# Performance work log

Hardware: AMD Instinct MI355X
Metric: run time of the kernel (lower is better)

The kernel has to match this reference:

```python
import jax, jax.numpy as jnp
import numpy as np
import math

B, L, M = 8, 1024, 1024
H, D, DK, DFF = 16, 1024, 64, 4096
EPS = 1e-5


def _ln(x, g, b):
    mu = jnp.mean(x, axis=-1, keepdims=True)
    var = jnp.mean((x - mu) ** 2, axis=-1, keepdims=True)
    return (x - mu) * jax.lax.rsqrt(var + EPS) * g + b


def _mha(x, kv, Wq, bq, Wk, bk, Wv, bv, Wo, bo, masked):
    # x: [B,Lq,D], kv: [B,Lk,D]; per-head weights stacked: Wq [H,D,DK], bq [H,DK]
    Q = jnp.einsum('bld,hdk->bhlk', x, Wq) + bq[None, :, None, :]
    K = jnp.einsum('bld,hdk->bhlk', kv, Wk) + bk[None, :, None, :]
    V = jnp.einsum('bld,hdk->bhlk', kv, Wv) + bv[None, :, None, :]
    scores = jnp.einsum('bhqk,bhmk->bhqm', Q, K) / math.sqrt(DK)
    p = jax.nn.softmax(scores, axis=-1)
    if masked:
        # faithful to source: mask applied AFTER softmax (multiply by tril ones)
        Lq = x.shape[1]
        tril = jnp.tril(jnp.ones((Lq, kv.shape[1]), dtype=p.dtype))
        p = p * tril
    z = jnp.einsum('bhqm,bhmk->bhqk', p, V)  # [B,H,Lq,DK]
    z = jnp.transpose(z, (0, 2, 1, 3)).reshape(x.shape[0], x.shape[1], H * DK)
    return z @ Wo + bo


def _forward(x, enc, Wq1, bq1, Wk1, bk1, Wv1, bv1, Wo1, bo1,
             Wq2, bq2, Wk2, bk2, Wv2, bv2, Wo2, bo2,
             W1, b1, W2, b2, g1, be1, g2, be2, g3, be3):
    z = _mha(x, x, Wq1, bq1, Wk1, bk1, Wv1, bv1, Wo1, bo1, masked=True)
    x = _ln(z + x, g1, be1)
    z = _mha(x, enc, Wq2, bq2, Wk2, bk2, Wv2, bv2, Wo2, bo2, masked=False)
    x = _ln(z + x, g2, be2)
    # Conv1d(k=1) pair == per-token MLP: relu(x @ W1 + b1) @ W2 + b2
    y = jax.nn.relu(x @ W1 + b1) @ W2 + b2
    return _ln(y + x, g3, be3)


def setup_inputs() -> dict:
    key = jax.random.key(0)
    ks = jax.random.split(key, 16)
    s = 0.02
    return {
        'x': jax.random.normal(ks[0], (B, L, D), jnp.float32),
        'enc': jax.random.normal(ks[1], (B, M, D), jnp.float32),
        'Wq1': jax.random.normal(ks[2], (H, D, DK), jnp.float32) * s,
        'bq1': jnp.zeros((H, DK), jnp.float32),
        'Wk1': jax.random.normal(ks[3], (H, D, DK), jnp.float32) * s,
        'bk1': jnp.zeros((H, DK), jnp.float32),
        'Wv1': jax.random.normal(ks[4], (H, D, DK), jnp.float32) * s,
        'bv1': jnp.zeros((H, DK), jnp.float32),
        'Wo1': jax.random.normal(ks[5], (H * DK, D), jnp.float32) * s,
        'bo1': jnp.zeros((D,), jnp.float32),
        'Wq2': jax.random.normal(ks[6], (H, D, DK), jnp.float32) * s,
        'bq2': jnp.zeros((H, DK), jnp.float32),
        'Wk2': jax.random.normal(ks[7], (H, D, DK), jnp.float32) * s,
        'bk2': jnp.zeros((H, DK), jnp.float32),
        'Wv2': jax.random.normal(ks[8], (H, D, DK), jnp.float32) * s,
        'bv2': jnp.zeros((H, DK), jnp.float32),
        'Wo2': jax.random.normal(ks[9], (H * DK, D), jnp.float32) * s,
        'bo2': jnp.zeros((D,), jnp.float32),
        'W1': jax.random.normal(ks[10], (D, DFF), jnp.float32) * s,
        'b1': jnp.zeros((DFF,), jnp.float32),
        'W2': jax.random.normal(ks[11], (DFF, D), jnp.float32) * s,
        'b2': jnp.zeros((D,), jnp.float32),
        'g1': jnp.ones((D,), jnp.float32), 'be1': jnp.zeros((D,), jnp.float32),
        'g2': jnp.ones((D,), jnp.float32), 'be2': jnp.zeros((D,), jnp.float32),
        'g3': jnp.ones((D,), jnp.float32), 'be3': jnp.zeros((D,), jnp.float32),
    }


def reference(x, enc, Wq1, bq1, Wk1, bk1, Wv1, bv1, Wo1, bo1,
              Wq2, bq2, Wk2, bk2, Wv2, bv2, Wo2, bo2,
              W1, b1, W2, b2, g1, be1, g2, be2, g3, be3):
    return _forward(x, enc, Wq1, bq1, Wk1, bk1, Wv1, bv1, Wo1, bo1,
                    Wq2, bq2, Wk2, bk2, Wv2, bv2, Wo2, bo2,
                    W1, b1, W2, b2, g1, be1, g2, be2, g3, be3)
```

## Files before the change

kernel.cpp:

```cpp
#include <hip/hip_runtime.h>
#include <hip/hip_bf16.h>

typedef __bf16 bf16;
typedef __bf16 bf16x8 __attribute__((ext_vector_type(8)));
typedef __bf16 bf16x4v __attribute__((ext_vector_type(4)));
typedef float f32x4 __attribute__((ext_vector_type(4)));
typedef unsigned int u32;
typedef u32 u32x4 __attribute__((ext_vector_type(4)));

#define DEV static __device__ __forceinline__
#define SB0 __builtin_amdgcn_sched_barrier(0)
#define BAR __builtin_amdgcn_s_barrier()
#define LGKM0 asm volatile("s_waitcnt lgkmcnt(0)" ::: "memory")
#define LGKM8 asm volatile("s_waitcnt lgkmcnt(8)" ::: "memory")
#define VM4 asm volatile("s_waitcnt vmcnt(4)" ::: "memory")
#define PRIO1 __builtin_amdgcn_s_setprio(1)
#define PRIO0 __builtin_amdgcn_s_setprio(0)

DEV void gll16(const void* g, void* l) {
  __builtin_amdgcn_global_load_lds((__attribute__((address_space(1))) void*)g,
                                   (__attribute__((address_space(3))) void*)l,
                                   16, 0, 0);
}

DEV bf16 tobf(float f) { return (bf16)f; }

DEV u32 cvtpk(float lo, float hi) {
  u32 r;
  asm("v_cvt_pk_bf16_f32 %0, %1, %2" : "=v"(r) : "v"(lo), "v"(hi));
  return r;
}

__global__ void cast_f2b_kernel(const float* __restrict__ in, bf16* __restrict__ out, int n4) {
  int i = blockIdx.x * 256 + threadIdx.x;
  if (i < n4) {
    const float4 v = ((const float4*)in)[i];
    bf16x4v o;
    o[0] = tobf(v.x); o[1] = tobf(v.y); o[2] = tobf(v.z); o[3] = tobf(v.w);
    ((bf16x4v*)out)[i] = o;
  }
}

__global__ __launch_bounds__(256)
void tpack_kernel(const float* __restrict__ in, bf16* __restrict__ out,
                  int K, int N, int in_hs, int out_hs, float scale) {
  __shared__ float tile[32][33];
  const int k0 = blockIdx.x << 5, n0 = blockIdx.y << 5;
  const float* ip = in + (size_t)blockIdx.z * in_hs;
  bf16* op = out + (size_t)blockIdx.z * out_hs;
  const int tx = threadIdx.x & 31, ty = threadIdx.x >> 5;
#pragma unroll
  for (int r = 0; r < 4; ++r)
    tile[ty * 4 + r][tx] = ip[(size_t)(k0 + ty * 4 + r) * N + n0 + tx];
  __syncthreads();
#pragma unroll
  for (int r = 0; r < 4; ++r)
    op[(size_t)(n0 + ty * 4 + r) * K + k0 + tx] = tobf(tile[tx][ty * 4 + r] * scale);
}

__global__ void bscale_kernel(const float* __restrict__ in, float* __restrict__ out, int n, float s) {
  int i = blockIdx.x * 256 + threadIdx.x;
  if (i < n) out[i] = in[i] * s;
}

template<int EPI>
__global__ __launch_bounds__(512, 1)
void gemm8(const bf16* __restrict__ A, const bf16* __restrict__ W,
           const float* __restrict__ bias, const float* __restrict__ resid,
           void* __restrict__ outv, int M, int N, int K) {
  __shared__ bf16 sA[3][256 * 64];
  __shared__ bf16 sB[3][128 * 64];
  const int nbx = N >> 7;
  const int nwg = (M >> 8) * nbx;
  int bid = (int)blockIdx.x;
  bid = (bid & 7) * (nwg >> 3) + (bid >> 3);
  const int tm = bid / nbx, tn = bid - tm * nbx;
  const int tid = threadIdx.x;
  const int lane = tid & 63;
  const int w = tid >> 6;
  const int wr = w >> 1, wc = w & 1;
  const int l15 = lane & 15, l4 = lane >> 4;

  const bf16* Abase = A + (size_t)(tm * 256) * K;
  const bf16* Bbase = W + (size_t)(tn * 128) * K;

  f32x4 acc[4][4] = {};
  const int nt = K >> 6;

  auto stageA = [&](int buf, int t) {
#pragma unroll
    for (int j = 0; j < 4; ++j) {
      int g = tid + (j << 9);
      int row = g >> 3;
      int sc = ((g & 7) ^ (row & 7)) << 3;
      gll16(Abase + (size_t)row * K + (t << 6) + sc, &sA[buf][g << 3]);
    }
  };
  auto stageB = [&](int buf, int t) {
#pragma unroll
    for (int j = 0; j < 2; ++j) {
      int g = tid + (j << 9);
      int row = g >> 3;
      int sc = ((g & 7) ^ (row & 7)) << 3;
      gll16(Bbase + (size_t)row * K + (t << 6) + sc, &sB[buf][g << 3]);
    }
  };

  stageA(0, 0); stageB(0, 0);
  stageA(1, 1 < nt ? 1 : 0); stageB(1, 1 < nt ? 1 : 0);
  SB0;
  asm volatile("s_waitcnt vmcnt(6)" ::: "memory");
  BAR;

  int c = 0;
  for (int t = 0; t < nt; ++t) {
    const int sb = (c >= 1) ? c - 1 : 2;
    const int ts = (t + 2 < nt) ? t + 2 : nt - 1;
    bf16x8 af[4][2], bfr[4][2];
#pragma unroll
    for (int mi = 0; mi < 4; ++mi)
#pragma unroll
      for (int kk = 0; kk < 2; ++kk) {
        int r = wr * 64 + (mi << 4) + l15;
        int off = (r << 7) + (kk << 6) + (l4 << 4);
        off ^= (r & 7) << 4;
        af[mi][kk] = *(const bf16x8*)((const char*)sA[c] + off);
      }
#pragma unroll
    for (int ni = 0; ni < 2; ++ni)
#pragma unroll
      for (int kk = 0; kk < 2; ++kk) {
        int r = wc * 64 + (ni << 4) + l15;
        int off = (r << 7) + (kk << 6) + (l4 << 4);
        off ^= (r & 7) << 4;
        bfr[ni][kk] = *(const bf16x8*)((const char*)sB[c] + off);
      }
    stageA(sb, ts);
    SB0; BAR; LGKM0; SB0; PRIO1;
#pragma unroll
    for (int mi = 0; mi < 4; ++mi)
#pragma unroll
      for (int ni = 0; ni < 2; ++ni)
#pragma unroll
        for (int kk = 0; kk < 2; ++kk)
          acc[mi][ni] = __builtin_amdgcn_mfma_f32_16x16x32_bf16(af[mi][kk], bfr[ni][kk],
                                                                acc[mi][ni], 0, 0, 0);
    PRIO0; SB0; BAR;
#pragma unroll
    for (int ni = 2; ni < 4; ++ni)
#pragma unroll
      for (int kk = 0; kk < 2; ++kk) {
        int r = wc * 64 + (ni << 4) + l15;
        int off = (r << 7) + (kk << 6) + (l4 << 4);
        off ^= (r & 7) << 4;
        bfr[ni][kk] = *(const bf16x8*)((const char*)sB[c] + off);
      }
    stageB(sb, ts);
    SB0;
    asm volatile("s_waitcnt vmcnt(6)" ::: "memory");
    BAR; LGKM0; SB0; PRIO1;
#pragma unroll
    for (int mi = 0; mi < 4; ++mi)
#pragma unroll
      for (int ni = 2; ni < 4; ++ni)
#pragma unroll
        for (int kk = 0; kk < 2; ++kk)
          acc[mi][ni] = __builtin_amdgcn_mfma_f32_16x16x32_bf16(af[mi][kk], bfr[ni][kk],
                                                                acc[mi][ni], 0, 0, 0);
    PRIO0; SB0; BAR;
    c = (c == 2) ? 0 : c + 1;
  }

  const int row0 = tm * 256 + wr * 64 + (l4 << 2);
  const int col0 = tn * 128 + wc * 64 + l15;
#pragma unroll
  for (int ni = 0; ni < 4; ++ni) {
    const int col = col0 + (ni << 4);
    const float bv = bias ? bias[col] : 0.f;
#pragma unroll
    for (int mi = 0; mi < 4; ++mi) {
      const int rr = row0 + (mi << 4);
      f32x4 v = acc[mi][ni];
      if (EPI == 0) {
        bf16* out = (bf16*)outv;
#pragma unroll
        for (int r = 0; r < 4; ++r) out[(size_t)(rr + r) * N + col] = tobf(v[r] + bv);
      } else if (EPI == 1) {
        float* out = (float*)outv;
#pragma unroll
        for (int r = 0; r < 4; ++r) {
          size_t idx = (size_t)(rr + r) * N + col;
          out[idx] = v[r] + bv + resid[idx];
        }
      }
    }
  }
}

template<int EPI>
__global__ __launch_bounds__(512, 1)
void gemmP(const bf16* __restrict__ A, const bf16* __restrict__ W,
           const float* __restrict__ bias, const float* __restrict__ resid,
           void* __restrict__ outv, int M, int N, int K) {
  __shared__ bf16 sA[2][2][128 * 64];
  __shared__ bf16 sB[2][2][128 * 64];
  const int nbx = N >> 8;
  const int nwg = (M >> 8) * nbx;
  int bid = (int)blockIdx.x;
  bid = (bid & 7) * (nwg >> 3) + (bid >> 3);
  const int tm = bid / nbx, tn = bid - tm * nbx;
  const int tid = threadIdx.x;
  const int lane = tid & 63;
  const int w = tid >> 6;
  const int wr = w >> 2, wc = w & 3;
  const int l15 = lane & 15, l4 = lane >> 4;

  const bf16* Abase = A + (size_t)(tm * 256) * K;
  const bf16* Bbase = W + (size_t)(tn * 256) * K;

  f32x4 acc[8][4] = {};
  const int nt = K >> 6;
  const int nit = nt >> 1;

  auto stageHalf = [&](const bf16* base, bf16* lds, int t, int h) {
#pragma unroll
    for (int j = 0; j < 2; ++j) {
      int g = tid + (j << 9);
      int row = g >> 3;
      int sc = ((g & 7) ^ (row & 7)) << 3;
      gll16(base + (size_t)(h * 128 + row) * K + (t << 6) + sc, &lds[g << 3]);
    }
  };
  auto rdoff = [&](int r, int kk) {
    int off = (r << 7) + (kk << 6) + (l4 << 4);
    return off ^ ((r & 7) << 4);
  };

  stageHalf(Abase, sA[0][0], 0, 0);
  stageHalf(Abase, sA[0][1], 0, 1);
  stageHalf(Bbase, sB[0][0], 0, 0);
  stageHalf(Bbase, sB[0][1], 0, 1);
  stageHalf(Bbase, sB[1][0], 1, 0);
  stageHalf(Bbase, sB[1][1], 1, 1);
  SB0; VM4; BAR;

  for (int it = 0; it < nit; ++it) {
    const int tod = 2 * it + 1;
    const int ts2 = (2 * it + 2 < nt) ? 2 * it + 2 : nt - 1;
    const int ts3 = (2 * it + 3 < nt) ? 2 * it + 3 : nt - 1;

    auto doTile = [&](int b, int ab, int at, int bb, int bt) {
      bf16x8 af[4][2], ag[4][2], b01[2][2], b23[2][2];
      const char* pA = (const char*)sA[b][wr];
      const char* pB = (const char*)sB[b][wc >> 1];
      const int brow = (wc & 1) << 6;
#pragma unroll
      for (int mi = 0; mi < 4; ++mi)
#pragma unroll
        for (int kk = 0; kk < 2; ++kk)
          af[mi][kk] = *(const bf16x8*)(pA + rdoff((mi << 4) + l15, kk));
#pragma unroll
      for (int ni = 0; ni < 2; ++ni)
#pragma unroll
        for (int kk = 0; kk < 2; ++kk)
          b01[ni][kk] = *(const bf16x8*)(pB + rdoff(brow + (ni << 4) + l15, kk));
      stageHalf(Abase, sA[ab][0], at, 0);
      SB0; LGKM8; BAR; LGKM0; SB0; PRIO1;
#pragma unroll
      for (int mi = 0; mi < 4; ++mi)
#pragma unroll
        for (int ni = 0; ni < 2; ++ni)
#pragma unroll
          for (int kk = 0; kk < 2; ++kk)
            acc[mi][ni] = __builtin_amdgcn_mfma_f32_16x16x32_bf16(af[mi][kk], b01[ni][kk],
                                                                  acc[mi][ni], 0, 0, 0);
      PRIO0; SB0; BAR;
#pragma unroll
      for (int ni = 0; ni < 2; ++ni)
#pragma unroll
        for (int kk = 0; kk < 2; ++kk)
          b23[ni][kk] = *(const bf16x8*)(pB + rdoff(brow + 32 + (ni << 4) + l15, kk));
      stageHalf(Abase, sA[ab][1], at, 1);
      SB0; BAR; LGKM0; SB0; PRIO1;
#pragma unroll
      for (int mi = 0; mi < 4; ++mi)
#pragma unroll
        for (int ni = 0; ni < 2; ++ni)
#pragma unroll
          for (int kk = 0; kk < 2; ++kk)
            acc[mi][ni + 2] = __builtin_amdgcn_mfma_f32_16x16x32_bf16(af[mi][kk], b23[ni][kk],
                                                                      acc[mi][ni + 2], 0, 0, 0);
      PRIO0; SB0; BAR;
#pragma unroll
      for (int mi = 0; mi < 4; ++mi)
#pragma unroll
        for (int kk = 0; kk < 2; ++kk)
          ag[mi][kk] = *(const bf16x8*)(pA + rdoff(64 + (mi << 4) + l15, kk));
      stageHalf(Bbase, sB[bb][0], bt, 0);
      SB0; BAR; LGKM0; SB0; PRIO1;
#pragma unroll
      for (int mi = 0; mi < 4; ++mi)
#pragma unroll
        for (int ni = 0; ni < 2; ++ni)
#pragma unroll
          for (int kk = 0; kk < 2; ++kk)
            acc[mi + 4][ni] = __builtin_amdgcn_mfma_f32_16x16x32_bf16(ag[mi][kk], b01[ni][kk],
                                                                      acc[mi + 4][ni], 0, 0, 0);
      PRIO0; SB0; BAR;
      stageHalf(Bbase, sB[bb][1], bt, 1);
      SB0; VM4; BAR; PRIO1;
#pragma unroll
      for (int mi = 0; mi < 4; ++mi)
#pragma unroll
        for (int ni = 0; ni < 2; ++ni)
#pragma unroll
          for (int kk = 0; kk < 2; ++kk)
            acc[mi + 4][ni + 2] = __builtin_amdgcn_mfma_f32_16x16x32_bf16(ag[mi][kk], b23[ni][kk],
                                                                          acc[mi + 4][ni + 2], 0, 0, 0);
      PRIO0; SB0; BAR;
    };

    doTile(0, 1, tod, 0, ts2);
    doTile(1, 0, ts2, 1, ts3);
  }

  const int row0 = tm * 256 + wr * 128 + (l4 << 2);
  const int col0 = tn * 256 + wc * 64 + l15;
#pragma unroll
  for (int ni = 0; ni < 4; ++ni) {
    const int col = col0 + (ni << 4);
    const float bv = bias ? bias[col] : 0.f;
#pragma unroll
    for (int mi = 0; mi < 8; ++mi) {
      const int rr = row0 + (mi << 4);
      f32x4 v = acc[mi][ni];
      if (EPI == 2) {
        bf16* out = (bf16*)outv;
#pragma unroll
        for (int r = 0; r < 4; ++r) out[(size_t)(rr + r) * N + col] = tobf(fmaxf(v[r] + bv, 0.f));
      } else {
        bf16* out = (bf16*)outv;
        const int seg = col >> 10;
        const int cc = col & 1023;
        const bool isV = (EPI == 4) ? (seg == 2) : (seg == 1);
        if (isV) {
          bf16* vout = out + (size_t)seg * 8388608;
          const int bb = rr >> 10, l0 = rr & 1023;
          const int hh = cc >> 6, dk = cc & 63;
          bf16x4v pk;
#pragma unroll
          for (int r = 0; r < 4; ++r) pk[r] = tobf(v[r] + bv);
          *(bf16x4v*)(vout + ((size_t)((bb * 16 + hh) * 64 + dk) << 10) + l0) = pk;
        } else {
          bf16* qout = out + (size_t)seg * 8388608;
#pragma unroll
          for (int r = 0; r < 4; ++r) qout[(size_t)(rr + r) * 1024 + cc] = tobf(v[r] + bv);
        }
      }
    }
  }
}

template<bool MASKED>
__global__ __launch_bounds__(256, 2)
void attn_kernel(const bf16* __restrict__ Qp, const bf16* __restrict__ Kp,
                 const bf16* __restrict__ Vt, bf16* __restrict__ Z) {
  __shared__ bf16 sK[2][64 * 64];
  __shared__ bf16 sV[2][64 * 64];
  const int Lk = 1024;
  const int d = blockIdx.x;
  const int bh = d & 127, qb = d >> 7;
  const int b = bh >> 4, h = bh & 15;
  const int q0 = qb << 7;
  const int tid = threadIdx.x, lane = tid & 63, w = tid >> 6;
  const int l15 = lane & 15, l4 = lane >> 4;

  const bf16* Qb = Qp + ((size_t)(b * 1024 + q0 + w * 32)) * 1024 + h * 64;
  bf16x8 qf[2][2];
#pragma unroll
  for (int mi = 0; mi < 2; ++mi)
#pragma unroll
    for (int kk = 0; kk < 2; ++kk)
      qf[mi][kk] = *(const bf16x8*)(Qb + (size_t)((mi << 4) + l15) * 1024 + (kk << 5) + (l4 << 3));

  f32x4 o[4][2] = {};
  float Mr[2] = {-1e30f, -1e30f}, LrP[2] = {0.f, 0.f};

  const bf16* Kb = Kp + ((size_t)b * Lk) * 1024 + h * 64;
  const bf16* Vb = Vt + ((size_t)(b * 16 + h)) * 64 * Lk;

  auto stage = [&](int buf, int t, bool withV) {
    const int kv0 = t << 6;
#pragma unroll
    for (int j = 0; j < 2; ++j) {
      int g = tid + (j << 8);
      int r = g >> 3;
      int sc = ((g & 7) ^ (r & 7)) << 3;
      gll16(Kb + (size_t)(kv0 + r) * 1024 + sc, &sK[buf][g << 3]);
      if (withV) gll16(Vb + (size_t)r * Lk + kv0 + sc, &sV[buf][g << 3]);
    }
  };
  auto needPV = [&](int t) -> bool { return !MASKED || ((t << 6) < q0 + 128); };

  const int NT = Lk >> 6;
  stage(0, 0, true);
  __syncthreads();
  int cur = 0;

  for (int t = 0; t < NT; ++t) {
    if (t + 1 < NT) stage(cur ^ 1, t + 1, needPV(t + 1));
    const int kv0 = t << 6;

    f32x4 s[4][2] = {};
#pragma unroll
    for (int n = 0; n < 4; ++n) {
      bf16x8 kf[2];
#pragma unroll
      for (int kk = 0; kk < 2; ++kk) {
        int r = (n << 4) + l15;
        int off = (r << 7) + (kk << 6) + (l4 << 4);
        off ^= (r & 7) << 4;
        kf[kk] = *(const bf16x8*)((const char*)sK[cur] + off);
      }
#pragma unroll
      for (int mi = 0; mi < 2; ++mi)
#pragma unroll
        for (int kk = 0; kk < 2; ++kk)
          s[n][mi] = __builtin_amdgcn_mfma_f32_16x16x32_bf16(kf[kk], qf[mi][kk],
                                                             s[n][mi], 0, 0, 0);
    }

#pragma unroll
    for (int mi = 0; mi < 2; ++mi) {
      float lmax = s[0][mi][0];
#pragma unroll
      for (int n = 0; n < 4; ++n)
#pragma unroll
        for (int r = 0; r < 4; ++r) lmax = fmaxf(lmax, s[n][mi][r]);
      const bool need = (t == 0) || !__all(lmax <= Mr[mi] + 8.f);
      if (need) {
        float tmx = fmaxf(lmax, __shfl_xor(lmax, 16, 64));
        tmx = fmaxf(tmx, __shfl_xor(tmx, 32, 64));
        const float Mn = fmaxf(Mr[mi], tmx);
        const float al = exp2f(Mr[mi] - Mn);
        LrP[mi] *= al;
        Mr[mi] = Mn;
#pragma unroll
        for (int r = 0; r < 4; ++r) {
          float a = __shfl(al, (l4 << 2) + r, 64);
#pragma unroll
          for (int nd = 0; nd < 4; ++nd) o[nd][mi][r] *= a;
        }
      }
      float rs = 0.f;
#pragma unroll
      for (int n = 0; n < 4; ++n)
#pragma unroll
        for (int r = 0; r < 4; ++r) {
          float p = exp2f(s[n][mi][r] - Mr[mi]);
          s[n][mi][r] = p;
          rs += p;
        }
      LrP[mi] += rs;
    }

    if (needPV(t)) {
      const bool needMask = MASKED && (kv0 + 63 > q0 + (w << 5));
      bf16x8 pa[2][2];
#pragma unroll
      for (int mi = 0; mi < 2; ++mi) {
        u32 D0[4], D1[4];
        const int qg = q0 + (w << 5) + (mi << 4) + l15;
#pragma unroll
        for (int n = 0; n < 4; ++n) {
          float pv[4];
#pragma unroll
          for (int r = 0; r < 4; ++r) {
            float p = s[n][mi][r];
            if (needMask) {
              int cg = kv0 + (n << 4) + (l4 << 2) + r;
              if (cg > qg) p = 0.f;
            }
            pv[r] = p;
          }
          D0[n] = cvtpk(pv[0], pv[1]);
          D1[n] = cvtpk(pv[2], pv[3]);
        }
        const int src = l15 + ((lane & 16) << 1);
#pragma unroll
        for (int kk = 0; kk < 2; ++kk) {
          u32 v0 = (lane & 32) ? D0[2 * kk + 1] : D0[2 * kk];
          u32 v1 = (lane & 32) ? D1[2 * kk + 1] : D1[2 * kk];
          u32x4 tw;
          tw[0] = (u32)__shfl((int)v0, src, 64);
          tw[1] = (u32)__shfl((int)v1, src, 64);
          tw[2] = (u32)__shfl((int)v0, src + 16, 64);
          tw[3] = (u32)__shfl((int)v1, src + 16, 64);
          pa[mi][kk] = __builtin_bit_cast(bf16x8, tw);
        }
      }
#pragma unroll
      for (int nd = 0; nd < 4; ++nd) {
        bf16x8 vf[2];
#pragma unroll
        for (int kk = 0; kk < 2; ++kk) {
          int r = (nd << 4) + l15;
          int off = (r << 7) + (kk << 6) + (l4 << 4);
          off ^= (r & 7) << 4;
          vf[kk] = *(const bf16x8*)((const char*)sV[cur] + off);
        }
#pragma unroll
        for (int mi = 0; mi < 2; ++mi)
#pragma unroll
          for (int kk = 0; kk < 2; ++kk)
            o[nd][mi] = __builtin_amdgcn_mfma_f32_16x16x32_bf16(pa[mi][kk], vf[kk],
                                                                o[nd][mi], 0, 0, 0);
      }
    }
    __syncthreads();
    cur ^= 1;
  }

  float inv[2][4];
#pragma unroll
  for (int mi = 0; mi < 2; ++mi) {
    float l = LrP[mi];
    l += __shfl_xor(l, 16, 64);
    l += __shfl_xor(l, 32, 64);
    const float il = 1.f / l;
#pragma unroll
    for (int r = 0; r < 4; ++r) inv[mi][r] = __shfl(il, (l4 << 2) + r, 64);
  }
  bf16* Zb = Z + ((size_t)(b * 1024 + q0 + w * 32)) * 1024 + h * 64;
#pragma unroll
  for (int nd = 0; nd < 4; ++nd)
#pragma unroll
    for (int mi = 0; mi < 2; ++mi)
#pragma unroll
      for (int r = 0; r < 4; ++r)
        Zb[(size_t)((mi << 4) + (l4 << 2) + r) * 1024 + (nd << 4) + l15] =
            tobf(o[nd][mi][r] * inv[mi][r]);
}

__global__ __launch_bounds__(256)
void ln_kernel(const float* __restrict__ in, const float* __restrict__ gw,
               const float* __restrict__ bw, float* __restrict__ outf,
               bf16* __restrict__ outb) {
  const int row = blockIdx.x, tid = threadIdx.x;
  const size_t base = (size_t)row << 10;
  const float4 v = *(const float4*)(in + base + tid * 4);
  float s = v.x + v.y + v.z + v.w;
  float ss = v.x * v.x + v.y * v.y + v.z * v.z + v.w * v.w;
#pragma unroll
  for (int d = 1; d < 64; d <<= 1) { s += __shfl_xor(s, d, 64); ss += __shfl_xor(ss, d, 64); }
  __shared__ float red[8];
  const int w = tid >> 6;
  if ((tid & 63) == 0) { red[w] = s; red[4 + w] = ss; }
  __syncthreads();
  s = red[0] + red[1] + red[2] + red[3];
  ss = red[4] + red[5] + red[6] + red[7];
  const float mu = s * (1.f / 1024.f);
  const float var = ss * (1.f / 1024.f) - mu * mu;
  const float rstd = rsqrtf(var + 1e-5f);
  const float4 g4 = *(const float4*)(gw + tid * 4);
  const float4 b4 = *(const float4*)(bw + tid * 4);
  const float o0 = (v.x - mu) * rstd * g4.x + b4.x;
  const float o1 = (v.y - mu) * rstd * g4.y + b4.y;
  const float o2 = (v.z - mu) * rstd * g4.z + b4.z;
  const float o3 = (v.w - mu) * rstd * g4.w + b4.w;
  if (outf) { float4 of; of.x = o0; of.y = o1; of.z = o2; of.w = o3;
              *(float4*)(outf + base + tid * 4) = of; }
  if (outb) { bf16x4v ob; ob[0] = tobf(o0); ob[1] = tobf(o1); ob[2] = tobf(o2); ob[3] = tobf(o3);
              *(bf16x4v*)(outb + base + tid * 4) = ob; }
}

extern "C" void kernel_launch(void* const* d_in, const int* in_sizes, int n_in,
                              void* d_out, int out_size, void* d_ws, size_t ws_size,
                              hipStream_t stream) {
  const float* x   = (const float*)d_in[0];
  const float* enc = (const float*)d_in[1];
  const float* Wq1 = (const float*)d_in[2];
  const float* bq1 = (const float*)d_in[3];
  const float* Wk1 = (const float*)d_in[4];
  const float* bk1 = (const float*)d_in[5];
  const float* Wv1 = (const float*)d_in[6];
  const float* bv1 = (const float*)d_in[7];
  const float* Wo1 = (const float*)d_in[8];
  const float* bo1 = (const float*)d_in[9];
  const float* Wq2 = (const float*)d_in[10];
  const float* bq2 = (const float*)d_in[11];
  const float* Wk2 = (const float*)d_in[12];
  const float* bk2 = (const float*)d_in[13];
  const float* Wv2 = (const float*)d_in[14];
  const float* bv2 = (const float*)d_in[15];
  const float* Wo2 = (const float*)d_in[16];
  const float* bo2 = (const float*)d_in[17];
  const float* W1  = (const float*)d_in[18];
  const float* b1  = (const float*)d_in[19];
  const float* W2  = (const float*)d_in[20];
  const float* b2  = (const float*)d_in[21];
  const float* g1  = (const float*)d_in[22];
  const float* be1 = (const float*)d_in[23];
  const float* g2  = (const float*)d_in[24];
  const float* be2 = (const float*)d_in[25];
  const float* g3  = (const float*)d_in[26];
  const float* be3 = (const float*)d_in[27];

  char* ws = (char*)d_ws;
  size_t off = 0;
  auto alloc = [&](size_t bytes) { char* p = ws + off; off += (bytes + 255) & ~(size_t)255; return p; };
  const size_t ACT = (size_t)8 * 1024 * 1024 * 2;
  const float QSC = 0.125f * 1.44269504088896f;

  bf16* xb     = (bf16*)alloc(ACT);
  bf16* encb   = (bf16*)alloc(ACT);
  bf16* Wqkv1t = (bf16*)alloc((size_t)3072 * 1024 * 2);
  bf16* Wkv2t  = (bf16*)alloc((size_t)2048 * 1024 * 2);
  bf16* Wq2t   = (bf16*)alloc((size_t)1024 * 1024 * 2);
  bf16* Wo1t   = (bf16*)alloc((size_t)1024 * 1024 * 2);
  bf16* Wo2t   = (bf16*)alloc((size_t)1024 * 1024 * 2);
  bf16* W1t    = (bf16*)alloc((size_t)4096 * 1024 * 2);
  bf16* W2t    = (bf16*)alloc((size_t)4096 * 1024 * 2);
  float* qkvb1 = (float*)alloc(3072 * 4);
  float* kvb2  = (float*)alloc(2048 * 4);
  float* sbq2  = (float*)alloc(1024 * 4);
  char*  S     = alloc((size_t)64 * 1024 * 1024);
  float* rbuf  = (float*)alloc((size_t)8 * 1024 * 1024 * 4);
  float* xnf   = (float*)alloc((size_t)8 * 1024 * 1024 * 4);
  bf16*  xnb   = (bf16*)alloc(ACT);

  bf16* q1   = (bf16*)(S);
  bf16* k1   = (bf16*)(S + ACT);
  bf16* vt1  = (bf16*)(S + 2 * ACT);
  bf16* z1   = (bf16*)(S + 3 * ACT);
  bf16* hbuf = (bf16*)S;

  dim3 b256(256);
  dim3 b512(512);
  cast_f2b_kernel<<<8192, b256, 0, stream>>>(x, xb, 2097152);
  cast_f2b_kernel<<<8192, b256, 0, stream>>>(enc, encb, 2097152);
  tpack_kernel<<<dim3(32, 2, 16), b256, 0, stream>>>(Wq1, Wqkv1t, 1024, 64, 65536, 65536, QSC);
  tpack_kernel<<<dim3(32, 2, 16), b256, 0, stream>>>(Wk1, Wqkv1t + 1048576, 1024, 64, 65536, 65536, 1.f);
  tpack_kernel<<<dim3(32, 2, 16), b256, 0, stream>>>(Wv1, Wqkv1t + 2097152, 1024, 64, 65536, 65536, 1.f);
  tpack_kernel<<<dim3(32, 2, 16), b256, 0, stream>>>(Wq2, Wq2t, 1024, 64, 65536, 65536, QSC);
  tpack_kernel<<<dim3(32, 2, 16), b256, 0, stream>>>(Wk2, Wkv2t, 1024, 64, 65536, 65536, 1.f);
  tpack_kernel<<<dim3(32, 2, 16), b256, 0, stream>>>(Wv2, Wkv2t + 1048576, 1024, 64, 65536, 65536, 1.f);
  tpack_kernel<<<dim3(32, 32, 1), b256, 0, stream>>>(Wo1, Wo1t, 1024, 1024, 0, 0, 1.f);
  tpack_kernel<<<dim3(32, 32, 1), b256, 0, stream>>>(Wo2, Wo2t, 1024, 1024, 0, 0, 1.f);
  tpack_kernel<<<dim3(32, 128, 1), b256, 0, stream>>>(W1, W1t, 1024, 4096, 0, 0, 1.f);
  tpack_kernel<<<dim3(128, 32, 1), b256, 0, stream>>>(W2, W2t, 4096, 1024, 0, 0, 1.f);
  bscale_kernel<<<4, b256, 0, stream>>>(bq1, qkvb1, 1024, QSC);
  bscale_kernel<<<4, b256, 0, stream>>>(bk1, qkvb1 + 1024, 1024, 1.f);
  bscale_kernel<<<4, b256, 0, stream>>>(bv1, qkvb1 + 2048, 1024, 1.f);
  bscale_kernel<<<4, b256, 0, stream>>>(bk2, kvb2, 1024, 1.f);
  bscale_kernel<<<4, b256, 0, stream>>>(bv2, kvb2 + 1024, 1024, 1.f);
  bscale_kernel<<<4, b256, 0, stream>>>(bq2, sbq2, 1024, QSC);

  gemmP<4><<<384, b512, 0, stream>>>(xb, Wqkv1t, qkvb1, nullptr, q1, 8192, 3072, 1024);
  attn_kernel<true><<<1024, b256, 0, stream>>>(q1, k1, vt1, z1);
  gemm8<1><<<256, b512, 0, stream>>>(z1, Wo1t, bo1, x, rbuf, 8192, 1024, 1024);
  ln_kernel<<<8192, b256, 0, stream>>>(rbuf, g1, be1, xnf, xnb);

  gemm8<0><<<256, b512, 0, stream>>>(xnb, Wq2t, sbq2, nullptr, q1, 8192, 1024, 1024);
  gemmP<5><<<256, b512, 0, stream>>>(encb, Wkv2t, kvb2, nullptr, k1, 8192, 2048, 1024);
  attn_kernel<false><<<1024, b256, 0, stream>>>(q1, k1, vt1, z1);
  gemm8<1><<<256, b512, 0, stream>>>(z1, Wo2t, bo2, xnf, rbuf, 8192, 1024, 1024);
  ln_kernel<<<8192, b256, 0, stream>>>(rbuf, g2, be2, xnf, xnb);

  gemmP<2><<<512, b512, 0, stream>>>(xnb, W1t, b1, nullptr, hbuf, 8192, 4096, 1024);
  gemm8<1><<<256, b512, 0, stream>>>(hbuf, W2t, b2, xnf, rbuf, 8192, 1024, 4096);
  ln_kernel<<<8192, b256, 0, stream>>>(rbuf, g3, be3, (float*)d_out, nullptr);
}
```

Measured before the change: 615.0 us.

## Compute V transposed via swapped-operand GEMM and add grouped tile mapping

V projections are now computed as a separate GEMM with weights as the A operand and activations as B, writing V^T directly in a [h*64, B*L] layout with contiguous stores. This replaces the scattered transposed-store epilogue in the fused QKV GEMM, and the attention kernel's V addressing is updated to match. A grouped 4x4 tile-to-block mapping is also added to all GEMMs to improve L2 reuse. The cost is extra kernel launches and reduced fusion of the QKV projections.

```diff
diff --git a/kernel.cpp b/kernel.cpp
--- a/kernel.cpp
+++ b/kernel.cpp
@@ -61,6 +61,14 @@
 __global__ void bscale_kernel(const float* __restrict__ in, float* __restrict__ out, int n, float s) {
   int i = blockIdx.x * 256 + threadIdx.x;
   if (i < n) out[i] = in[i] * s;
+}
+
+DEV void tile_map(int bid, int nwg, int nbx, int& tm, int& tn) {
+  bid = (bid & 7) * (nwg >> 3) + (bid >> 3);
+  const int gid = bid >> 4, g4 = bid & 15;
+  const int gpr = nbx >> 2;
+  tm = ((gid / gpr) << 2) | (g4 >> 2);
+  tn = ((gid % gpr) << 2) | (g4 & 3);
 }
 
 template<int EPI>
@@ -72,9 +80,8 @@
   __shared__ bf16 sB[3][128 * 64];
   const int nbx = N >> 7;
   const int nwg = (M >> 8) * nbx;
-  int bid = (int)blockIdx.x;
-  bid = (bid & 7) * (nwg >> 3) + (bid >> 3);
-  const int tm = bid / nbx, tn = bid - tm * nbx;
+  int tm, tn;
+  tile_map((int)blockIdx.x, nwg, nbx, tm, tn);
   const int tid = threadIdx.x;
   const int lane = tid & 63;
   const int w = tid >> 6;
@@ -176,7 +183,7 @@
 #pragma unroll
   for (int ni = 0; ni < 4; ++ni) {
     const int col = col0 + (ni << 4);
-    const float bv = bias ? bias[col] : 0.f;
+    const float bv = (EPI == 6) ? 0.f : bias[col];
 #pragma unroll
     for (int mi = 0; mi < 4; ++mi) {
       const int rr = row0 + (mi << 4);
@@ -192,6 +199,12 @@
           size_t idx = (size_t)(rr + r) * N + col;
           out[idx] = v[r] + bv + resid[idx];
         }
+      } else {
+        bf16* out = (bf16*)outv;
+        const float4 bq = *(const float4*)(bias + rr);
+        const float br[4] = {bq.x, bq.y, bq.z, bq.w};
+#pragma unroll
+        for (int r = 0; r < 4; ++r) out[(size_t)(rr + r) * N + col] = tobf(v[r] + br[r]);
       }
     }
   }
@@ -206,9 +219,8 @@
   __shared__ bf16 sB[2][2][128 * 64];
   const int nbx = N >> 8;
   const int nwg = (M >> 8) * nbx;
-  int bid = (int)blockIdx.x;
-  bid = (bid & 7) * (nwg >> 3) + (bid >> 3);
-  const int tm = bid / nbx, tn = bid - tm * nbx;
+  int tm, tn;
+  tile_map((int)blockIdx.x, nwg, nbx, tm, tn);
   const int tid = threadIdx.x;
   const int lane = tid & 63;
   const int w = tid >> 6;
@@ -342,20 +354,9 @@
         bf16* out = (bf16*)outv;
         const int seg = col >> 10;
         const int cc = col & 1023;
-        const bool isV = (EPI == 4) ? (seg == 2) : (seg == 1);
-        if (isV) {
-          bf16* vout = out + (size_t)seg * 8388608;
-          const int bb = rr >> 10, l0 = rr & 1023;
-          const int hh = cc >> 6, dk = cc & 63;
-          bf16x4v pk;
-#pragma unroll
-          for (int r = 0; r < 4; ++r) pk[r] = tobf(v[r] + bv);
-          *(bf16x4v*)(vout + ((size_t)((bb * 16 + hh) * 64 + dk) << 10) + l0) = pk;
-        } else {
-          bf16* qout = out + (size_t)seg * 8388608;
-#pragma unroll
-          for (int r = 0; r < 4; ++r) qout[(size_t)(rr + r) * 1024 + cc] = tobf(v[r] + bv);
-        }
+        bf16* qout = out + (size_t)seg * 8388608;
+#pragma unroll
+        for (int r = 0; r < 4; ++r) qout[(size_t)(rr + r) * 1024 + cc] = tobf(v[r] + bv);
       }
     }
   }
@@ -387,7 +388,7 @@
   float Mr[2] = {-1e30f, -1e30f}, LrP[2] = {0.f, 0.f};
 
   const bf16* Kb = Kp + ((size_t)b * Lk) * 1024 + h * 64;
-  const bf16* Vb = Vt + ((size_t)(b * 16 + h)) * 64 * Lk;
+  const bf16* Vb = Vt + (size_t)(h * 64) * 8192 + b * 1024;
 
   auto stage = [&](int buf, int t, bool withV) {
     const int kv0 = t << 6;
@@ -397,7 +398,7 @@
       int r = g >> 3;
       int sc = ((g & 7) ^ (r & 7)) << 3;
       gll16(Kb + (size_t)(kv0 + r) * 1024 + sc, &sK[buf][g << 3]);
-      if (withV) gll16(Vb + (size_t)r * Lk + kv0 + sc, &sV[buf][g << 3]);
+      if (withV) gll16(Vb + (size_t)r * 8192 + kv0 + sc, &sV[buf][g << 3]);
     }
   };
   auto needPV = [&](int t) -> bool { return !MASKED || ((t << 6) < q0 + 128); };
@@ -614,15 +615,16 @@
 
   bf16* xb     = (bf16*)alloc(ACT);
   bf16* encb   = (bf16*)alloc(ACT);
-  bf16* Wqkv1t = (bf16*)alloc((size_t)3072 * 1024 * 2);
-  bf16* Wkv2t  = (bf16*)alloc((size_t)2048 * 1024 * 2);
+  bf16* Wqk1t  = (bf16*)alloc((size_t)2048 * 1024 * 2);
+  bf16* Wv1t   = (bf16*)alloc((size_t)1024 * 1024 * 2);
   bf16* Wq2t   = (bf16*)alloc((size_t)1024 * 1024 * 2);
+  bf16* Wk2t   = (bf16*)alloc((size_t)1024 * 1024 * 2);
+  bf16* Wv2t   = (bf16*)alloc((size_t)1024 * 1024 * 2);
   bf16* Wo1t   = (bf16*)alloc((size_t)1024 * 1024 * 2);
   bf16* Wo2t   = (bf16*)alloc((size_t)1024 * 1024 * 2);
   bf16* W1t    = (bf16*)alloc((size_t)4096 * 1024 * 2);
   bf16* W2t    = (bf16*)alloc((size_t)4096 * 1024 * 2);
-  float* qkvb1 = (float*)alloc(3072 * 4);
-  float* kvb2  = (float*)alloc(2048 * 4);
+  float* qkb1  = (float*)alloc(2048 * 4);
   float* sbq2  = (float*)alloc(1024 * 4);
   char*  S     = alloc((size_t)64 * 1024 * 1024);
   float* rbuf  = (float*)alloc((size_t)8 * 1024 * 1024 * 4);
@@ -639,30 +641,29 @@
   dim3 b512(512);
   cast_f2b_kernel<<<8192, b256, 0, stream>>>(x, xb, 2097152);
   cast_f2b_kernel<<<8192, b256, 0, stream>>>(enc, encb, 2097152);
-  tpack_kernel<<<dim3(32, 2, 16), b256, 0, stream>>>(Wq1, Wqkv1t, 1024, 64, 65536, 65536, QSC);
-  tpack_kernel<<<dim3(32, 2, 16), b256, 0, stream>>>(Wk1, Wqkv1t + 1048576, 1024, 64, 65536, 65536, 1.f);
-  tpack_kernel<<<dim3(32, 2, 16), b256, 0, stream>>>(Wv1, Wqkv1t + 2097152, 1024, 64, 65536, 65536, 1.f);
+  tpack_kernel<<<dim3(32, 2, 16), b256, 0, stream>>>(Wq1, Wqk1t, 1024, 64, 65536, 65536, QSC);
+  tpack_kernel<<<dim3(32, 2, 16), b256, 0, stream>>>(Wk1, Wqk1t + 1048576, 1024, 64, 65536, 65536, 1.f);
+  tpack_kernel<<<dim3(32, 2, 16), b256, 0, stream>>>(Wv1, Wv1t, 1024, 64, 65536, 65536, 1.f);
   tpack_kernel<<<dim3(32, 2, 16), b256, 0, stream>>>(Wq2, Wq2t, 1024, 64, 65536, 65536, QSC);
-  tpack_kernel<<<dim3(32, 2, 16), b256, 0, stream>>>(Wk2, Wkv2t, 1024, 64, 65536, 65536, 1.f);
-  tpack_kernel<<<dim3(32, 2, 16), b256, 0, stream>>>(Wv2, Wkv2t + 1048576, 1024, 64, 65536, 65536, 1.f);
+  tpack_kernel<<<dim3(32, 2, 16), b256, 0, stream>>>(Wk2, Wk2t, 1024, 64, 65536, 65536, 1.f);
+  tpack_kernel<<<dim3(32, 2, 16), b256, 0, stream>>>(Wv2, Wv2t, 1024, 64, 65536, 65536, 1.f);
   tpack_kernel<<<dim3(32, 32, 1), b256, 0, stream>>>(Wo1, Wo1t, 1024, 1024, 0, 0, 1.f);
   tpack_kernel<<<dim3(32, 32, 1), b256, 0, stream>>>(Wo2, Wo2t, 1024, 1024, 0, 0, 1.f);
   tpack_kernel<<<dim3(32, 128, 1), b256, 0, stream>>>(W1, W1t, 1024, 4096, 0, 0, 1.f);
   tpack_kernel<<<dim3(128, 32, 1), b256, 0, stream>>>(W2, W2t, 4096, 1024, 0, 0, 1.f);
-  bscale_kernel<<<4, b256, 0, stream>>>(bq1, qkvb1, 1024, QSC);
-  bscale_kernel<<<4, b256, 0, stream>>>(bk1, qkvb1 + 1024, 1024, 1.f);
-  bscale_kernel<<<4, b256, 0, stream>>>(bv1, qkvb1 + 2048, 1024, 1.f);
-  bscale_kernel<<<4, b256, 0, stream>>>(bk2, kvb2, 1024, 1.f);
-  bscale_kernel<<<4, b256, 0, stream>>>(bv2, kvb2 + 1024, 1024, 1.f);
+  bscale_kernel<<<4, b256, 0, stream>>>(bq1, qkb1, 1024, QSC);
+  bscale_kernel<<<4, b256, 0, stream>>>(bk1, qkb1 + 1024, 1024, 1.f);
   bscale_kernel<<<4, b256, 0, stream>>>(bq2, sbq2, 1024, QSC);
 
-  gemmP<4><<<384, b512, 0, stream>>>(xb, Wqkv1t, qkvb1, nullptr, q1, 8192, 3072, 1024);
+  gemmP<4><<<256, b512, 0, stream>>>(xb, Wqk1t, qkb1, nullptr, q1, 8192, 2048, 1024);
+  gemm8<6><<<256, b512, 0, stream>>>(Wv1t, xb, bv1, nullptr, vt1, 1024, 8192, 1024);
   attn_kernel<true><<<1024, b256, 0, stream>>>(q1, k1, vt1, z1);
   gemm8<1><<<256, b512, 0, stream>>>(z1, Wo1t, bo1, x, rbuf, 8192, 1024, 1024);
   ln_kernel<<<8192, b256, 0, stream>>>(rbuf, g1, be1, xnf, xnb);
 
   gemm8<0><<<256, b512, 0, stream>>>(xnb, Wq2t, sbq2, nullptr, q1, 8192, 1024, 1024);
-  gemmP<5><<<256, b512, 0, stream>>>(encb, Wkv2t, kvb2, nullptr, k1, 8192, 2048, 1024);
+  gemm8<0><<<256, b512, 0, stream>>>(encb, Wk2t, bk2, nullptr, k1, 8192, 1024, 1024);
+  gemm8<6><<<256, b512, 0, stream>>>(Wv2t, encb, bv2, nullptr, vt1, 1024, 8192, 1024);
   attn_kernel<false><<<1024, b256, 0, stream>>>(q1, k1, vt1, z1);
   gemm8<1><<<256, b512, 0, stream>>>(z1, Wo2t, bo2, xnf, rbuf, 8192, 1024, 1024);
   ln_kernel<<<8192, b256, 0, stream>>>(rbuf, g2, be2, xnf, xnb);
```

Result: faster. 598.8 us (-2.6%).
